# Optimization experiments

Hardware: AMD Instinct MI355X
Metric: run time of the kernel (lower is better)

The kernel has to match this reference:

```python
import jax, jax.numpy as jnp
import numpy as np
import math

B, S, E, H = 2, 1024, 2560, 32
D = E // H  # 80


def setup_inputs() -> dict:
    key = jax.random.key(0)
    ks = jax.random.split(key, 10)
    hidden_states = jax.random.normal(ks[0], (B, S, E), dtype=jnp.float32)
    Wqkv = jax.random.normal(ks[1], (E, 3 * E), dtype=jnp.float32) * 0.02
    bqkv = jnp.zeros((3 * E,), dtype=jnp.float32)
    Wproj = jax.random.normal(ks[2], (E, E), dtype=jnp.float32) * 0.02
    bproj = jnp.zeros((E,), dtype=jnp.float32)
    # gate matrices: hadamard, pauli_x, pauli_z (all real branches in torch code)
    hadamard = jnp.array([[1.0, 1.0], [1.0, -1.0]], dtype=jnp.float32) / math.sqrt(2.0)
    pauli_x = jnp.array([[0.0, 1.0], [1.0, 0.0]], dtype=jnp.float32)
    pauli_z = jnp.array([[1.0, 0.0], [0.0, -1.0]], dtype=jnp.float32)
    gate_mats = jnp.stack([hadamard, pauli_x, pauli_z])  # (3,2,2)
    # phase_rotation init is zeros in torch; randomize slightly for nontrivial numerics
    gate_phases = jax.random.normal(ks[3], (3, D), dtype=jnp.float32) * 0.1
    gate_amps = jnp.ones((3, D), dtype=jnp.float32)
    quantum_phase = jax.random.normal(ks[4], (H,), dtype=jnp.float32) * 0.1
    interference_strength = jnp.float32(0.8)
    return {
        'hidden_states': hidden_states, 'Wqkv': Wqkv, 'bqkv': bqkv,
        'Wproj': Wproj, 'bproj': bproj, 'gate_mats': gate_mats,
        'gate_phases': gate_phases, 'gate_amps': gate_amps,
        'quantum_phase': quantum_phase,
        'interference_strength': interference_strength,
    }


def _gate_coeffs(gate_mats, gate_phases, gate_amps):
    # QuantumGate fwd: stack([x*cos(p), x*sin(p)], -1) @ G, summed over last axis, * amp
    # => per-dim scalar coeff: (cos(p)*(g00+g01) + sin(p)*(g10+g11)) * amp
    row0 = gate_mats[:, 0, 0] + gate_mats[:, 0, 1]  # (3,)
    row1 = gate_mats[:, 1, 0] + gate_mats[:, 1, 1]  # (3,)
    return (jnp.cos(gate_phases) * row0[:, None] + jnp.sin(gate_phases) * row1[:, None]) * gate_amps  # (3, D)


def reference(hidden_states, Wqkv, bqkv, Wproj, bproj, gate_mats, gate_phases, gate_amps, quantum_phase, interference_strength):
    scale = D ** -0.5
    qkv = hidden_states @ Wqkv + bqkv  # (B,S,3E)
    q, k, v = jnp.split(qkv, 3, axis=-1)
    # (B,H,S,D)
    q = q.reshape(B, S, H, D).transpose(0, 2, 1, 3)
    k = k.reshape(B, S, H, D).transpose(0, 2, 1, 3)
    v = v.reshape(B, S, H, D).transpose(0, 2, 1, 3)

    attn_scores = jnp.einsum('bhqd,bhkd->bhqk', q, k) * scale

    coeffs = _gate_coeffs(gate_mats, gate_phases, gate_amps)  # (3,D)
    # quantum attention per gate: (q * coeff_i) @ k^T * scale
    qa = jnp.einsum('gd,bhqd,bhkd->gbhqk', coeffs, q, k) * scale  # (3,B,H,S,S)
    interference = (qa[0] * qa[1] + qa[0] * qa[2] + qa[1] * qa[2]) * interference_strength
    attn_scores = attn_scores + interference / 3.0

    attn_probs = jax.nn.softmax(attn_scores, axis=-1)
    attn_probs = attn_probs * jnp.cos(quantum_phase)[None, :, None, None]

    attn_output = jnp.einsum('bhqk,bhkd->bhqd', attn_probs, v)
    attn_output = attn_output.transpose(0, 2, 1, 3).reshape(B, S, E)
    return attn_output @ Wproj + bproj
```

## Files before the change

### kernel.cpp

```cpp
#include <hip/hip_runtime.h>
#include <hip/hip_bf16.h>
#include <math.h>

#define S_  1024
#define E_  2560
#define H_  32
#define D_  80
#define E3_ 7680
#define M_  2048
#define QK_ 5120

typedef short bf16x8 __attribute__((ext_vector_type(8)));
typedef float f32x4  __attribute__((ext_vector_type(4)));

static __device__ __forceinline__ float bf2f(unsigned short u) {
    unsigned int i = ((unsigned int)u) << 16;
    float f; __builtin_memcpy(&f, &i, 4); return f;
}
static __device__ __forceinline__ unsigned short f2bf(float f) {
    unsigned int i; __builtin_memcpy(&i, &f, 4);
    i += 0x7fffu + ((i >> 16) & 1u);
    return (unsigned short)(i >> 16);
}

static __device__ __forceinline__ void gload_lds16(
    const unsigned short* g, unsigned short* l)
{
    __builtin_amdgcn_global_load_lds(
        (const __attribute__((address_space(1))) void*)g,
        (__attribute__((address_space(3))) void*)l, 16, 0, 0);
}

__global__ __launch_bounds__(256) void cvt_bf16_kernel(
    const float* __restrict__ in, unsigned short* __restrict__ out, int n8)
{
    int i = (blockIdx.x * 256 + threadIdx.x);
    if (i >= n8) return;
    const float* p = in + (size_t)i * 8;
    float4 a = *(const float4*)p;
    float4 b = *(const float4*)(p + 4);
    union { uint4 v; unsigned short s[8]; } o;
    o.s[0]=f2bf(a.x); o.s[1]=f2bf(a.y); o.s[2]=f2bf(a.z); o.s[3]=f2bf(a.w);
    o.s[4]=f2bf(b.x); o.s[5]=f2bf(b.y); o.s[6]=f2bf(b.z); o.s[7]=f2bf(b.w);
    *(uint4*)(out + (size_t)i * 8) = o.v;
}

__global__ __launch_bounds__(256) void transpose_bf16_kernel(
    const float* __restrict__ in, unsigned short* __restrict__ out, int R, int C)
{
    const int t = threadIdx.x;
    const int r0 = blockIdx.y * 64, c0 = blockIdx.x * 64;
    const int r4 = (t >> 4) * 4;
    const int c4 = (t & 15) * 4;
    float4 rows[4];
#pragma unroll
    for (int i = 0; i < 4; ++i)
        rows[i] = *(const float4*)&in[(size_t)(r0 + r4 + i) * C + c0 + c4];
    const float rv[4][4] = {
        {rows[0].x, rows[0].y, rows[0].z, rows[0].w},
        {rows[1].x, rows[1].y, rows[1].z, rows[1].w},
        {rows[2].x, rows[2].y, rows[2].z, rows[2].w},
        {rows[3].x, rows[3].y, rows[3].z, rows[3].w}};
#pragma unroll
    for (int j = 0; j < 4; ++j) {
        ushort4 o;
        o.x = f2bf(rv[0][j]); o.y = f2bf(rv[1][j]);
        o.z = f2bf(rv[2][j]); o.w = f2bf(rv[3][j]);
        *(ushort4*)&out[(size_t)(c0 + c4 + j) * R + r0 + r4] = o;
    }
}

template <bool OUT_F32>
__global__ __launch_bounds__(256) void mfma_gemm_kernel(
    const unsigned short* __restrict__ A, int lda,
    const unsigned short* __restrict__ Wt,
    const float* __restrict__ bias,
    void* __restrict__ dst0, int sd0,
    void* __restrict__ dst1, int sd1, int ncut,
    int K)
{
    __shared__ unsigned short As[2][128 * 32];
    __shared__ unsigned short Bs[2][128 * 32];
    const int BUFSZ = 128 * 32;

    const int t    = threadIdx.x;
    const int m0   = blockIdx.y * 128;
    const int n0   = blockIdx.x * 128;
    const int lane = t & 63, wave = t >> 6;
    const int quad = lane >> 4, l15 = lane & 15;
    const int mw   = (wave >> 1) * 64;
    const int nw   = (wave & 1) * 64;

    f32x4 acc[4][4];
#pragma unroll
    for (int i = 0; i < 4; ++i)
#pragma unroll
        for (int j = 0; j < 4; ++j) acc[i][j] = (f32x4){0.f, 0.f, 0.f, 0.f};

    const int srow  = lane >> 2;
    const int sslot = (lane & 3) * 8;

    const unsigned short* gA0 = A  + (size_t)(m0 + wave * 32 + srow) * lda + sslot;
    const unsigned short* gA1 = gA0 + (size_t)16 * lda;
    const unsigned short* gB0 = Wt + (size_t)(n0 + wave * 32 + srow) * K + sslot;
    const unsigned short* gB1 = gB0 + (size_t)16 * K;
    unsigned short* lA0 = &As[0][(wave * 32) * 32];
    unsigned short* lA1 = lA0 + 16 * 32;
    unsigned short* lB0 = &Bs[0][(wave * 32) * 32];
    unsigned short* lB1 = lB0 + 16 * 32;

    gload_lds16(gA0, lA0);
    gload_lds16(gA1, lA1);
    gload_lds16(gB0, lB0);
    gload_lds16(gB1, lB1);
    __syncthreads();

    int cur = 0;
    for (int k0 = 0; k0 < K; k0 += 32) {
        const int nxt = cur ^ 1;
        if (k0 + 32 < K) {
            gload_lds16(gA0 + k0 + 32, lA0 + nxt * BUFSZ);
            gload_lds16(gA1 + k0 + 32, lA1 + nxt * BUFSZ);
            gload_lds16(gB0 + k0 + 32, lB0 + nxt * BUFSZ);
            gload_lds16(gB1 + k0 + 32, lB1 + nxt * BUFSZ);
        }

        const unsigned short* rA = &As[cur][0];
        const unsigned short* rB = &Bs[cur][0];
        bf16x8 af[4], bfr[4];
#pragma unroll
        for (int i = 0; i < 4; ++i)
            af[i] = *(const bf16x8*)&rA[(mw + i * 16 + l15) * 32 + quad * 8];
#pragma unroll
        for (int j = 0; j < 4; ++j)
            bfr[j] = *(const bf16x8*)&rB[(nw + j * 16 + l15) * 32 + quad * 8];
#pragma unroll
        for (int i = 0; i < 4; ++i)
#pragma unroll
            for (int j = 0; j < 4; ++j)
                acc[i][j] = __builtin_amdgcn_mfma_f32_16x16x32_bf16(af[i], bfr[j], acc[i][j], 0, 0, 0);

        __syncthreads();
        cur = nxt;
    }

#pragma unroll
    for (int j = 0; j < 4; ++j) {
        const int col = n0 + nw + j * 16 + l15;
        const float bv = bias[col];
        if (OUT_F32) {
            float* dst = (float*)dst0;
#pragma unroll
            for (int i = 0; i < 4; ++i) {
                const int rowb = m0 + mw + i * 16 + quad * 4;
#pragma unroll
                for (int g = 0; g < 4; ++g)
                    dst[(size_t)(rowb + g) * sd0 + col] = acc[i][j][g] + bv;
            }
        } else {
            unsigned short* dst; int sd, cc;
            if (col < ncut) { dst = (unsigned short*)dst0; sd = sd0; cc = col; }
            else            { dst = (unsigned short*)dst1; sd = sd1; cc = col - ncut; }
#pragma unroll
            for (int i = 0; i < 4; ++i) {
                const int rowb = m0 + mw + i * 16 + quad * 4;
#pragma unroll
                for (int g = 0; g < 4; ++g)
                    dst[(size_t)(rowb + g) * sd + cc] = f2bf(acc[i][j][g] + bv);
            }
        }
    }
}

__global__ __launch_bounds__(256, 2) void attn_mfma_kernel(
    unsigned short* __restrict__ qk,
    const unsigned short* __restrict__ vsrc,
    const float* __restrict__ gmats,
    const float* __restrict__ gphases,
    const float* __restrict__ gamps,
    const float* __restrict__ qphase,
    const float* __restrict__ is_ptr)
{
    __shared__ unsigned short Ks[64 * 104];
    __shared__ unsigned short Vt[80 * 72];
    __shared__ unsigned short Ps[64 * 72];
    __shared__ float cs[240];

    const int t    = threadIdx.x;
    const int wave = t >> 6, lane = t & 63;
    const int quad = lane >> 4, l15 = lane & 15;
    const int lin0 = blockIdx.x;
    const int lin  = ((lin0 & 7) << 7) | (lin0 >> 3);
    const int qt = lin & 15;
    const int bh = lin >> 4;
    const int h  = bh & 31;
    const int b  = bh >> 5;

    const float scale = 0.111803398874989485f;
    const float c2    = scale * scale * is_ptr[0] * (1.0f / 3.0f);
    const float cosph = cosf(qphase[h]);

    if (t < 240) {
        int g = t / 80;
        float r0 = gmats[g*4+0] + gmats[g*4+1];
        float r1 = gmats[g*4+2] + gmats[g*4+3];
        cs[t] = (cosf(gphases[t]) * r0 + sinf(gphases[t]) * r1) * gamps[t];
    }

    const int srow = t >> 2;
    const int scg  = (t & 3) * 20;

    const int vkg  = t & 15;
    const int vdg0 = t >> 4;

    {
        const unsigned short* qp = qk + (size_t)(b * S_ + qt * 64 + srow) * QK_ + h * D_ + scg;
#pragma unroll
        for (int u = 0; u < 5; ++u)
            *(ushort4*)&Ks[srow * 104 + scg + 4 * u] = *(const ushort4*)(qp + 4 * u);
        *(ushort4*)&Ks[srow * 104 + 80 + (t & 3) * 4] = (ushort4){0, 0, 0, 0};
    }
    __syncthreads();

    ushort4 kpre[5];
    ushort4 vpre[8];
    {
        const unsigned short* kp = qk + (size_t)(b * S_ + srow) * QK_ + E_ + h * D_ + scg;
#pragma unroll
        for (int u = 0; u < 5; ++u) kpre[u] = *(const ushort4*)(kp + 4 * u);
        const unsigned short* vb = vsrc + (size_t)(b * S_) * E_ + h * D_;
#pragma unroll
        for (int i = 0; i < 4; ++i)
            vpre[i] = *(const ushort4*)(vb + (size_t)(vkg * 4 + i) * E_ + vdg0 * 4);
        if (t < 64) {
#pragma unroll
            for (int i = 0; i < 4; ++i)
                vpre[4 + i] = *(const ushort4*)(vb + (size_t)(vkg * 4 + i) * E_ + 64 + vdg0 * 4);
        }
    }

    bf16x8 afq[3], afg[3][3];
#pragma unroll
    for (int kc = 0; kc < 3; ++kc)
        afq[kc] = *(const bf16x8*)&Ks[(wave * 16 + l15) * 104 + quad * 8 + kc * 32];
#pragma unroll
    for (int g = 0; g < 3; ++g)
#pragma unroll
        for (int kc = 0; kc < 3; ++kc)
#pragma unroll
            for (int j = 0; j < 8; ++j) {
                int d = kc * 32 + quad * 8 + j;
                float c = (d < 80) ? cs[g * 80 + d] : 0.f;
                afg[g][kc][j] = (short)f2bf(bf2f((unsigned short)afq[kc][j]) * c);
            }

    f32x4 Ov[5];
#pragma unroll
    for (int nf = 0; nf < 5; ++nf) Ov[nf] = (f32x4){0.f, 0.f, 0.f, 0.f};
    float m_r[4] = {-INFINITY, -INFINITY, -INFINITY, -INFINITY};
    float l_r[4] = {0.f, 0.f, 0.f, 0.f};

    for (int kt = 0; kt < 16; ++kt) {
        __syncthreads();

#pragma unroll
        for (int u = 0; u < 5; ++u)
            *(ushort4*)&Ks[srow * 104 + scg + 4 * u] = kpre[u];

        {
            const unsigned short rm[4][4] = {
                {vpre[0].x, vpre[0].y, vpre[0].z, vpre[0].w},
                {vpre[1].x, vpre[1].y, vpre[1].z, vpre[1].w},
                {vpre[2].x, vpre[2].y, vpre[2].z, vpre[2].w},
                {vpre[3].x, vpre[3].y, vpre[3].z, vpre[3].w}};
#pragma unroll
            for (int j = 0; j < 4; ++j) {
                ushort4 w = {rm[0][j], rm[1][j], rm[2][j], rm[3][j]};
                *(ushort4*)&Vt[(vdg0 * 4 + j) * 72 + vkg * 4] = w;
            }
        }
        if (t < 64) {
            const unsigned short rm[4][4] = {
                {vpre[4].x, vpre[4].y, vpre[4].z, vpre[4].w},
                {vpre[5].x, vpre[5].y, vpre[5].z, vpre[5].w},
                {vpre[6].x, vpre[6].y, vpre[6].z, vpre[6].w},
                {vpre[7].x, vpre[7].y, vpre[7].z, vpre[7].w}};
#pragma unroll
            for (int j = 0; j < 4; ++j) {
                ushort4 w = {rm[0][j], rm[1][j], rm[2][j], rm[3][j]};
                *(ushort4*)&Vt[(64 + vdg0 * 4 + j) * 72 + vkg * 4] = w;
            }
        }
        __syncthreads();

        if (kt < 15) {
            const unsigned short* kp = qk + (size_t)(b * S_ + (kt + 1) * 64 + srow) * QK_ + E_ + h * D_ + scg;
#pragma unroll
            for (int u = 0; u < 5; ++u) kpre[u] = *(const ushort4*)(kp + 4 * u);
            const unsigned short* vb = vsrc + (size_t)(b * S_ + (kt + 1) * 64) * E_ + h * D_;
#pragma unroll
            for (int i = 0; i < 4; ++i)
                vpre[i] = *(const ushort4*)(vb + (size_t)(vkg * 4 + i) * E_ + vdg0 * 4);
            if (t < 64) {
#pragma unroll
                for (int i = 0; i < 4; ++i)
                    vpre[4 + i] = *(const ushort4*)(vb + (size_t)(vkg * 4 + i) * E_ + 64 + vdg0 * 4);
            }
        }

        float p[4][4];
        float mx[4] = {-INFINITY, -INFINITY, -INFINITY, -INFINITY};
#pragma unroll
        for (int hf = 0; hf < 2; ++hf) {
            f32x4 sacc[4][2];
#pragma unroll
            for (int v = 0; v < 4; ++v)
#pragma unroll
                for (int n = 0; n < 2; ++n) sacc[v][n] = (f32x4){0.f, 0.f, 0.f, 0.f};
#pragma unroll
            for (int kc = 0; kc < 3; ++kc) {
                bf16x8 bk[2];
#pragma unroll
                for (int n = 0; n < 2; ++n)
                    bk[n] = *(const bf16x8*)&Ks[((hf * 2 + n) * 16 + l15) * 104 + quad * 8 + kc * 32];
#pragma unroll
                for (int n = 0; n < 2; ++n)
                    sacc[0][n] = __builtin_amdgcn_mfma_f32_16x16x32_bf16(afq[kc], bk[n], sacc[0][n], 0, 0, 0);
#pragma unroll
                for (int g = 0; g < 3; ++g)
#pragma unroll
                    for (int n = 0; n < 2; ++n)
                        sacc[1+g][n] = __builtin_amdgcn_mfma_f32_16x16x32_bf16(afg[g][kc], bk[n], sacc[1+g][n], 0, 0, 0);
            }
#pragma unroll
            for (int n = 0; n < 2; ++n)
#pragma unroll
                for (int r = 0; r < 4; ++r) {
                    float s0 = sacc[1][n][r], s1 = sacc[2][n][r], s2 = sacc[3][n][r];
                    float s = fmaf(fmaf(s0, s1, (s0 + s1) * s2), c2, sacc[0][n][r] * scale);
                    p[hf * 2 + n][r] = s;
                    mx[r] = fmaxf(mx[r], s);
                }
        }

#pragma unroll
        for (int r = 0; r < 4; ++r) {
            mx[r] = fmaxf(mx[r], __shfl_xor(mx[r], 1));
            mx[r] = fmaxf(mx[r], __shfl_xor(mx[r], 2));
            mx[r] = fmaxf(mx[r], __shfl_xor(mx[r], 4));
            mx[r] = fmaxf(mx[r], __shfl_xor(mx[r], 8));
        }
        float alpha[4];
#pragma unroll
        for (int r = 0; r < 4; ++r) {
            float m_new = fmaxf(m_r[r], mx[r]);
            alpha[r] = __expf(m_r[r] - m_new);
            m_r[r] = m_new;
        }
#pragma unroll
        for (int nf = 0; nf < 4; ++nf)
#pragma unroll
            for (int r = 0; r < 4; ++r)
                p[nf][r] = __expf(p[nf][r] - m_r[r]);
#pragma unroll
        for (int r = 0; r < 4; ++r) {
            float s = p[0][r] + p[1][r] + p[2][r] + p[3][r];
            s += __shfl_xor(s, 1);
            s += __shfl_xor(s, 2);
            s += __shfl_xor(s, 4);
            s += __shfl_xor(s, 8);
            l_r[r] = l_r[r] * alpha[r] + s;
        }

#pragma unroll
        for (int nf = 0; nf < 4; ++nf)
#pragma unroll
            for (int r = 0; r < 4; ++r)
                Ps[(wave * 16 + quad * 4 + r) * 72 + l15 + 16 * nf] = f2bf(p[nf][r]);
        __asm__ volatile("s_waitcnt lgkmcnt(0)" ::: "memory");

#pragma unroll
        for (int nf = 0; nf < 5; ++nf)
#pragma unroll
            for (int r = 0; r < 4; ++r) Ov[nf][r] *= alpha[r];

        bf16x8 ap[2];
#pragma unroll
        for (int kc = 0; kc < 2; ++kc)
            ap[kc] = *(const bf16x8*)&Ps[(wave * 16 + l15) * 72 + quad * 8 + kc * 32];
#pragma unroll
        for (int nf = 0; nf < 5; ++nf)
#pragma unroll
            for (int kc = 0; kc < 2; ++kc) {
                bf16x8 bv = *(const bf16x8*)&Vt[(nf * 16 + l15) * 72 + quad * 8 + kc * 32];
                Ov[nf] = __builtin_amdgcn_mfma_f32_16x16x32_bf16(ap[kc], bv, Ov[nf], 0, 0, 0);
            }
    }

    float inv[4];
#pragma unroll
    for (int r = 0; r < 4; ++r) inv[r] = cosph / l_r[r];
#pragma unroll
    for (int nf = 0; nf < 5; ++nf)
#pragma unroll
        for (int r = 0; r < 4; ++r)
            qk[(size_t)(b * S_ + qt * 64 + wave * 16 + quad * 4 + r) * QK_ + h * D_ + nf * 16 + l15]
                = f2bf(Ov[nf][r] * inv[r]);
}

extern "C" void kernel_launch(void* const* d_in, const int* in_sizes, int n_in,
                              void* d_out, int out_size, void* d_ws, size_t ws_size,
                              hipStream_t stream) {
    (void)in_sizes; (void)n_in; (void)out_size; (void)ws_size;
    const float* hidden  = (const float*)d_in[0];
    const float* Wqkv    = (const float*)d_in[1];
    const float* bqkv    = (const float*)d_in[2];
    const float* Wproj   = (const float*)d_in[3];
    const float* bproj   = (const float*)d_in[4];
    const float* gmats   = (const float*)d_in[5];
    const float* gphases = (const float*)d_in[6];
    const float* gamps   = (const float*)d_in[7];
    const float* qphase  = (const float*)d_in[8];
    const float* is_ptr  = (const float*)d_in[9];

    unsigned short* qk_ws  = (unsigned short*)d_ws;
    unsigned short* h_bf16 = (unsigned short*)((char*)d_ws + (size_t)M_ * QK_ * 2);
    unsigned short* Wt     = (unsigned short*)((char*)d_ws + (size_t)M_ * QK_ * 2 + (size_t)M_ * E_ * 2);
    unsigned short* v_buf  = (unsigned short*)d_out;

    dim3 blk(256);
    cvt_bf16_kernel<<<dim3((M_ * E_ / 8 + 255) / 256), blk, 0, stream>>>(hidden, h_bf16, M_ * E_ / 8);
    transpose_bf16_kernel<<<dim3(E3_/64, E_/64), blk, 0, stream>>>(Wqkv, Wt, E_, E3_);
    mfma_gemm_kernel<false><<<dim3(E3_/128, M_/128), blk, 0, stream>>>(
        h_bf16, E_, Wt, bqkv, qk_ws, QK_, v_buf, E_, QK_, E_);
    attn_mfma_kernel<<<dim3(2 * H_ * (S_/64)), blk, 0, stream>>>(
        qk_ws, v_buf, gmats, gphases, gamps, qphase, is_ptr);
    transpose_bf16_kernel<<<dim3(E_/64, E_/64), blk, 0, stream>>>(Wproj, Wt, E_, E_);
    mfma_gemm_kernel<true><<<dim3(E_/128, M_/128), blk, 0, stream>>>(
        qk_ws, QK_, Wt, bproj, d_out, E_, d_out, E_, E_, E_);
}
```

Before: 455.6 us.

## Use 256x256-tile 512-thread MFMA GEMM for the QKV projection

Adds a new GEMM kernel with 256x256 output tiles, 8 waves, a K-step of 64, swizzled LDS layout and direct global-to-LDS double buffering, and uses it for the QKV projection. Larger tiles raise arithmetic intensity and cut redundant global loads, and the swizzle avoids LDS bank conflicts. The trade-offs are a grid of only 30x8=240 blocks, which may underfill the GPU, plus heavy register and LDS use (128 KB of LDS per block).

New measurement: 418.3 us. 8.2% less time.

```diff
diff --git a/kernel.cpp b/kernel.cpp
--- a/kernel.cpp
+++ b/kernel.cpp
@@ -67,6 +67,100 @@
         o.x = f2bf(rv[0][j]); o.y = f2bf(rv[1][j]);
         o.z = f2bf(rv[2][j]); o.w = f2bf(rv[3][j]);
         *(ushort4*)&out[(size_t)(c0 + c4 + j) * R + r0 + r4] = o;
+    }
+}
+
+__global__ __launch_bounds__(512, 2) void mfma_gemm256_kernel(
+    const unsigned short* __restrict__ A, int lda,
+    const unsigned short* __restrict__ Wt,
+    const float* __restrict__ bias,
+    unsigned short* __restrict__ dst0, int sd0,
+    unsigned short* __restrict__ dst1, int sd1, int ncut,
+    int K)
+{
+    __shared__ unsigned short lds[2][2][256 * 64];
+
+    const int t    = threadIdx.x;
+    const int lane = t & 63, wave = t >> 6;
+    const int quad = lane >> 4, l15 = lane & 15;
+    const int wm   = wave >> 2, wn = wave & 3;
+    const int m0   = blockIdx.y * 256;
+    const int n0   = blockIdx.x * 256;
+
+    const int pr = lane >> 3;
+    const int ls = ((lane & 7) - pr) & 7;
+    const unsigned short* gA[4];
+    const unsigned short* gB[4];
+#pragma unroll
+    for (int i = 0; i < 4; ++i) {
+        const int r = wave * 32 + i * 8 + pr;
+        gA[i] = A  + (size_t)(m0 + r) * lda + ls * 8;
+        gB[i] = Wt + (size_t)(n0 + r) * K   + ls * 8;
+    }
+
+    f32x4 acc[8][4];
+#pragma unroll
+    for (int mf = 0; mf < 8; ++mf)
+#pragma unroll
+        for (int nf = 0; nf < 4; ++nf) acc[mf][nf] = (f32x4){0.f, 0.f, 0.f, 0.f};
+
+#pragma unroll
+    for (int i = 0; i < 4; ++i) {
+        gload_lds16(gA[i], &lds[0][0][(wave * 32 + i * 8) * 64]);
+        gload_lds16(gB[i], &lds[0][1][(wave * 32 + i * 8) * 64]);
+    }
+
+    const int NT = K / 64;
+    for (int kt = 0; kt < NT; ++kt) {
+        __syncthreads();
+
+        if (kt + 1 < NT) {
+            const int nb = (kt + 1) & 1;
+            const size_t koff = (size_t)(kt + 1) * 64;
+#pragma unroll
+            for (int i = 0; i < 4; ++i) {
+                gload_lds16(gA[i] + koff, &lds[nb][0][(wave * 32 + i * 8) * 64]);
+                gload_lds16(gB[i] + koff, &lds[nb][1][(wave * 32 + i * 8) * 64]);
+            }
+        }
+
+        const unsigned short* As = &lds[kt & 1][0][0];
+        const unsigned short* Bs = &lds[kt & 1][1][0];
+#pragma unroll
+        for (int kc = 0; kc < 2; ++kc) {
+            bf16x8 bfr[4];
+#pragma unroll
+            for (int nf = 0; nf < 4; ++nf) {
+                const int row = wn * 64 + nf * 16 + l15;
+                const int ps  = (quad + 4 * kc + (row & 7)) & 7;
+                bfr[nf] = *(const bf16x8*)&Bs[row * 64 + ps * 8];
+            }
+#pragma unroll
+            for (int mf = 0; mf < 8; ++mf) {
+                const int row = wm * 128 + mf * 16 + l15;
+                const int ps  = (quad + 4 * kc + (row & 7)) & 7;
+                const bf16x8 af = *(const bf16x8*)&As[row * 64 + ps * 8];
+#pragma unroll
+                for (int nf = 0; nf < 4; ++nf)
+                    acc[mf][nf] = __builtin_amdgcn_mfma_f32_16x16x32_bf16(af, bfr[nf], acc[mf][nf], 0, 0, 0);
+            }
+        }
+    }
+
+#pragma unroll
+    for (int nf = 0; nf < 4; ++nf) {
+        const int col = n0 + wn * 64 + nf * 16 + l15;
+        const float bv = bias[col];
+        unsigned short* dst; int sd, cc;
+        if (col < ncut) { dst = dst0; sd = sd0; cc = col; }
+        else            { dst = dst1; sd = sd1; cc = col - ncut; }
+#pragma unroll
+        for (int mf = 0; mf < 8; ++mf) {
+            const int rowb = m0 + wm * 128 + mf * 16 + quad * 4;
+#pragma unroll
+            for (int g = 0; g < 4; ++g)
+                dst[(size_t)(rowb + g) * sd + cc] = f2bf(acc[mf][nf][g] + bv);
+        }
     }
 }
 
@@ -431,7 +525,7 @@
     dim3 blk(256);
     cvt_bf16_kernel<<<dim3((M_ * E_ / 8 + 255) / 256), blk, 0, stream>>>(hidden, h_bf16, M_ * E_ / 8);
     transpose_bf16_kernel<<<dim3(E3_/64, E_/64), blk, 0, stream>>>(Wqkv, Wt, E_, E3_);
-    mfma_gemm_kernel<false><<<dim3(E3_/128, M_/128), blk, 0, stream>>>(
+    mfma_gemm256_kernel<<<dim3(E3_/256, M_/256), dim3(512), 0, stream>>>(
         h_bf16, E_, Wt, bqkv, qk_ws, QK_, v_buf, E_, QK_, E_);
     attn_mfma_kernel<<<dim3(2 * H_ * (S_/64)), blk, 0, stream>>>(
         qk_ws, v_buf, gmats, gphases, gamps, qphase, is_ptr);
```
